# Kernel tuning notes

Hardware: AMD Instinct MI355X
Metric: run time of the kernel (lower is better)

## Reference

```python
import jax, jax.numpy as jnp
import numpy as np

KDIM = 8192
EPS = 1e-8  # F.cosine_similarity default eps


def _encoder(x, W1, b1, W2, b2, W3, b3):
    # x: [..., KDIM] -> [..., 128]; Linear(KDIM,512)->ReLU->Linear(512,256)->ReLU->Linear(256,128)
    h = jax.nn.relu(x @ W1 + b1)
    h = jax.nn.relu(h @ W2 + b2)
    return h @ W3 + b3


def setup_inputs() -> dict:
    key = jax.random.key(0)
    ks = jax.random.split(key, 16)

    def lin(k, fan_in, fan_out):
        bound = 1.0 / np.sqrt(fan_in)
        kw, kb = jax.random.split(k)
        W = jax.random.uniform(kw, (fan_in, fan_out), jnp.float32, -bound, bound)
        b = jax.random.uniform(kb, (fan_out,), jnp.float32, -bound, bound)
        return W, b

    W1, b1 = lin(ks[0], KDIM, 512)
    W2, b2 = lin(ks[1], 512, 256)
    W3, b3 = lin(ks[2], 256, 128)
    Wi1, bi1 = lin(ks[3], 128 + 6, 64)
    Wi2, bi2 = lin(ks[4], 64, 32)
    Wi3, bi3 = lin(ks[5], 32, 1)

    return {
        "new_knowledge": jax.random.normal(ks[6], (KDIM,), jnp.float32),
        "existing_knowledge": jax.random.normal(ks[7], (10, KDIM), jnp.float32),
        "math_metrics": jax.random.uniform(ks[8], (6,), jnp.float32),
        "W1": W1, "b1": b1, "W2": W2, "b2": b2, "W3": W3, "b3": b3,
        "Wi1": Wi1, "bi1": bi1, "Wi2": Wi2, "bi2": bi2, "Wi3": Wi3, "bi3": bi3,
    }


def reference(new_knowledge, existing_knowledge, math_metrics,
              W1, b1, W2, b2, W3, b3, Wi1, bi1, Wi2, bi2, Wi3, bi3):
    # Encode new knowledge: [128]
    new_enc = _encoder(new_knowledge, W1, b1, W2, b2, W3, b3)
    # Batched encode of the (up to 10) existing knowledge vectors: [10, 128]
    ex_enc = _encoder(existing_knowledge, W1, b1, W2, b2, W3, b3)

    # Per-item geometric distance (L2 norm of difference)
    diff = new_enc[None, :] - ex_enc                     # [10, 128]
    geo_dist = jnp.sqrt(jnp.sum(diff * diff, axis=-1))   # [10]

    # Per-item cosine similarity with torch eps clamping
    new_n = jnp.maximum(jnp.linalg.norm(new_enc), EPS)
    ex_n = jnp.maximum(jnp.linalg.norm(ex_enc, axis=-1), EPS)  # [10]
    cos = (ex_enc @ new_enc) / (new_n * ex_n)            # [10]

    avg_consistency = jnp.mean(geo_dist - cos)

    # Mathematical-constraint integrator MLP on [128 + 6]
    combined = jnp.concatenate([new_enc, math_metrics])  # [134]
    h = jax.nn.relu(combined @ Wi1 + bi1)
    h = jax.nn.relu(h @ Wi2 + bi2)
    quality = h @ Wi3 + bi3                              # [1]

    integration_loss = jnp.exp(-quality)                 # [1]
    total = jnp.squeeze(avg_consistency + integration_loss)
    return total
```

## Files before the change

### kernel.cpp

```cpp
#include <hip/hip_runtime.h>
#include <math.h>

#define EPS 1e-8f

__device__ __forceinline__ void gridbar(int* bar, int target) {
  __syncthreads();
  if (threadIdx.x == 0) {
    __threadfence();
    __hip_atomic_fetch_add(bar, 1, __ATOMIC_RELAXED, __HIP_MEMORY_SCOPE_AGENT);
    while (__hip_atomic_load(bar, __ATOMIC_RELAXED, __HIP_MEMORY_SCOPE_AGENT) < target) {
      __builtin_amdgcn_s_sleep(1);
    }
    __threadfence();
  }
  __syncthreads();
}

__device__ __forceinline__ float wredsum(float v) {
#pragma unroll
  for (int o = 32; o > 0; o >>= 1) v += __shfl_down(v, o, 64);
  return v;
}

__global__ __launch_bounds__(256) void k_l1(const float* __restrict__ xn,
                                            const float* __restrict__ xe,
                                            const float* __restrict__ W1,
                                            float* __restrict__ p1,
                                            int* __restrict__ bars) {
  if (blockIdx.x == 0 && blockIdx.y == 0 && threadIdx.x == 0) {
    bars[0] = 0; bars[1] = 0; bars[2] = 0;
  }
  __shared__ float red[11 * 16 * 65];
  const int cg  = threadIdx.x & 15;
  const int ks  = threadIdx.x >> 4;
  const int col = blockIdx.x * 64 + cg * 4;
  const int k0  = blockIdx.y * 256 + ks * 16;

  float4 acc[11];
#pragma unroll
  for (int r = 0; r < 11; ++r) acc[r] = make_float4(0.f, 0.f, 0.f, 0.f);

#pragma unroll 8
  for (int i = 0; i < 16; ++i) {
    const int k = k0 + i;
    const float4 w = *(const float4*)&W1[(size_t)k * 512 + col];
    float xv = xn[k];
    acc[0].x = fmaf(xv, w.x, acc[0].x); acc[0].y = fmaf(xv, w.y, acc[0].y);
    acc[0].z = fmaf(xv, w.z, acc[0].z); acc[0].w = fmaf(xv, w.w, acc[0].w);
#pragma unroll
    for (int r = 0; r < 10; ++r) {
      const float xr = xe[r * 8192 + k];
      acc[r + 1].x = fmaf(xr, w.x, acc[r + 1].x);
      acc[r + 1].y = fmaf(xr, w.y, acc[r + 1].y);
      acc[r + 1].z = fmaf(xr, w.z, acc[r + 1].z);
      acc[r + 1].w = fmaf(xr, w.w, acc[r + 1].w);
    }
  }

#pragma unroll
  for (int r = 0; r < 11; ++r) {
    const int base = (r * 16 + ks) * 65 + cg * 4;
    red[base]     = acc[r].x; red[base + 1] = acc[r].y;
    red[base + 2] = acc[r].z; red[base + 3] = acc[r].w;
  }
  __syncthreads();
  if (threadIdx.x < 176) {
    const int r = threadIdx.x >> 4;
    const int c = threadIdx.x & 15;
    float4 s = make_float4(0.f, 0.f, 0.f, 0.f);
#pragma unroll
    for (int k = 0; k < 16; ++k) {
      const int b = (r * 16 + k) * 65 + c * 4;
      s.x += red[b]; s.y += red[b + 1]; s.z += red[b + 2]; s.w += red[b + 3];
    }
    *(float4*)&p1[((size_t)blockIdx.y * 11 + r) * 512 + blockIdx.x * 64 + c * 4] = s;
  }
}

__global__ __launch_bounds__(256) void k_rest(
    const float* __restrict__ p1, const float* __restrict__ b1,
    const float* __restrict__ W2, const float* __restrict__ b2,
    const float* __restrict__ W3, const float* __restrict__ b3,
    const float* __restrict__ mm,
    const float* __restrict__ Wi1, const float* __restrict__ bi1,
    const float* __restrict__ Wi2, const float* __restrict__ bi2,
    const float* __restrict__ Wi3, const float* __restrict__ bi3,
    float* __restrict__ H1, float* __restrict__ H2a, float* __restrict__ enca,
    int* __restrict__ bars, float* __restrict__ out) {
  __shared__ float red2[11 * 16 * 17];
  __shared__ float red3[11 * 64 * 5];
  __shared__ __align__(16) float wi1s[134 * 64];
  __shared__ float comb[134];
  __shared__ float h1s[64];
  const int tid = threadIdx.x;
  const int b = blockIdx.x;

  if (tid < 88) {
    const int idx = b * 88 + tid;
    const int c = idx & 511;
    float s = b1[c];
#pragma unroll 8
    for (int ch = 0; ch < 32; ++ch) s += p1[(size_t)ch * 5632 + idx];
    H1[idx] = fmaxf(s, 0.f);
  } else if (tid < 132) {
    H2a[b * 44 + (tid - 88)] = 0.f;
  } else if (tid < 154) {
    enca[b * 22 + (tid - 132)] = 0.f;
  }
  gridbar(&bars[0], 64);

  {
    const int ct = b & 15, kt = b >> 4;
    const int c = tid & 15, ksl = tid >> 4;
    const int col = ct * 16 + c;
    float acc[11];
#pragma unroll
    for (int r = 0; r < 11; ++r) acc[r] = 0.f;
#pragma unroll
    for (int kk = 0; kk < 8; ++kk) {
      const int k = kt * 128 + kk * 16 + ksl;
      const float wv = W2[(size_t)k * 256 + col];
#pragma unroll
      for (int r = 0; r < 11; ++r) acc[r] = fmaf(H1[r * 512 + k], wv, acc[r]);
    }
#pragma unroll
    for (int r = 0; r < 11; ++r) red2[(r * 16 + ksl) * 17 + c] = acc[r];
  }
  __syncthreads();
  if (tid < 176) {
    const int r = tid >> 4, c = tid & 15;
    float s = 0.f;
#pragma unroll
    for (int ks = 0; ks < 16; ++ks) s += red2[(r * 16 + ks) * 17 + c];
    atomicAdd(&H2a[r * 256 + (b & 15) * 16 + c], s);
  }
  gridbar(&bars[1], 64);

  {
    const int ct = b & 31, kt = b >> 5;
    const int c = tid & 3, ksl = tid >> 2;
    const int col = ct * 4 + c;
    float acc[11];
#pragma unroll
    for (int r = 0; r < 11; ++r) acc[r] = 0.f;
#pragma unroll
    for (int kk = 0; kk < 2; ++kk) {
      const int k = kt * 128 + kk * 64 + ksl;
      const float wv = W3[(size_t)k * 128 + col];
      const float bb = b2[k];
#pragma unroll
      for (int r = 0; r < 11; ++r) {
        const float h2 = fmaxf(H2a[r * 256 + k] + bb, 0.f);
        acc[r] = fmaf(h2, wv, acc[r]);
      }
    }
#pragma unroll
    for (int r = 0; r < 11; ++r) red3[(r * 64 + ksl) * 5 + c] = acc[r];
  }
  __syncthreads();
  if (tid < 44) {
    const int r = tid >> 2, c = tid & 3;
    float s = 0.f;
#pragma unroll 8
    for (int ks = 0; ks < 64; ++ks) s += red3[(r * 64 + ks) * 5 + c];
    atomicAdd(&enca[r * 128 + (b & 31) * 4 + c], s);
  }
  gridbar(&bars[2], 64);
  if (b != 0) return;

  for (int i = tid; i < (134 * 64) / 4; i += 256)
    *(float4*)&wi1s[i * 4] = *(const float4*)&Wi1[i * 4];

  const int t = tid;
  float n0 = 0.f, n1 = 0.f, consist = 0.f, nn = 0.f;
  if (t < 64) {
    n0 = enca[t] + b3[t];
    n1 = enca[64 + t] + b3[64 + t];
    comb[t] = n0; comb[64 + t] = n1;
    if (t < 6) comb[128 + t] = mm[t];
    nn = wredsum(n0 * n0 + n1 * n1);
#pragma unroll
    for (int r = 1; r <= 10; ++r) {
      const float e0 = enca[r * 128 + t] + b3[t];
      const float e1 = enca[r * 128 + 64 + t] + b3[64 + t];
      const float d0 = e0 - n0, d1 = e1 - n1;
      const float g  = wredsum(d0 * d0 + d1 * d1);
      const float q  = wredsum(e0 * e0 + e1 * e1);
      const float dd = wredsum(e0 * n0 + e1 * n1);
      if (t == 0) {
        const float geo = sqrtf(g);
        const float den = fmaxf(sqrtf(nn), EPS) * fmaxf(sqrtf(q), EPS);
        consist += geo - dd / den;
      }
    }
  }
  __syncthreads();
  if (t < 64) {
    float h = bi1[t];
#pragma unroll 4
    for (int k = 0; k < 134; ++k) h = fmaf(comb[k], wi1s[k * 64 + t], h);
    h1s[t] = fmaxf(h, 0.f);
  }
  __syncthreads();
  if (t < 64) {
    float part = 0.f;
    if (t < 32) {
      float h2 = bi2[t];
#pragma unroll 8
      for (int k = 0; k < 64; ++k) h2 = fmaf(h1s[k], Wi2[k * 32 + t], h2);
      part = fmaxf(h2, 0.f) * Wi3[t];
    }
    const float qual = wredsum(part);
    if (t == 0) out[0] = consist * 0.1f + expf(-(qual + bi3[0]));
  }
}

extern "C" void kernel_launch(void* const* d_in, const int* in_sizes, int n_in,
                              void* d_out, int out_size, void* d_ws, size_t ws_size,
                              hipStream_t stream) {
  (void)in_sizes; (void)n_in; (void)out_size; (void)ws_size;
  const float* xn  = (const float*)d_in[0];
  const float* xe  = (const float*)d_in[1];
  const float* mm  = (const float*)d_in[2];
  const float* W1  = (const float*)d_in[3];
  const float* b1  = (const float*)d_in[4];
  const float* W2  = (const float*)d_in[5];
  const float* b2  = (const float*)d_in[6];
  const float* W3  = (const float*)d_in[7];
  const float* b3  = (const float*)d_in[8];
  const float* Wi1 = (const float*)d_in[9];
  const float* bi1 = (const float*)d_in[10];
  const float* Wi2 = (const float*)d_in[11];
  const float* bi2 = (const float*)d_in[12];
  const float* Wi3 = (const float*)d_in[13];
  const float* bi3 = (const float*)d_in[14];
  float* out = (float*)d_out;

  char* ws = (char*)d_ws;
  float* p1   = (float*)(ws);
  float* H1   = (float*)(ws + 720896);
  float* H2a  = (float*)(ws + 743424);
  float* enca = (float*)(ws + 754688);
  int*   bars = (int*)  (ws + 760320);

  hipLaunchKernelGGL(k_l1, dim3(8, 32), dim3(256), 0, stream, xn, xe, W1, p1, bars);
  hipLaunchKernelGGL(k_rest, dim3(64), dim3(256), 0, stream,
                     p1, b1, W2, b2, W3, b3, mm,
                     Wi1, bi1, Wi2, bi2, Wi3, bi3,
                     H1, H2a, enca, bars, out);
}
```

Measured before the change: 131.9 us.

## Replace grid-barrier persistent kernel with separate per-layer kernel launches

Drops the persistent 64-block kernel, with its software grid barriers and atomic accumulation, and splits the work into three kernels: H1 reduction, layer 2 (16 blocks, H1 staged in shared memory, no atomics) and a single 1024-thread block that does layer 3 plus the heads. The aim is to remove spin-wait barrier latency and atomic traffic, and to overlap the Wi1 load with the W3 matmul. The cost is two extra kernel launches and fewer blocks in the later stages, so parallelism there is lower.

Measured after the change: 120.6 us. 8.6% less time.

```diff
diff --git a/kernel.cpp b/kernel.cpp
--- a/kernel.cpp
+++ b/kernel.cpp
@@ -2,19 +2,6 @@
 #include <math.h>
 
 #define EPS 1e-8f
-
-__device__ __forceinline__ void gridbar(int* bar, int target) {
-  __syncthreads();
-  if (threadIdx.x == 0) {
-    __threadfence();
-    __hip_atomic_fetch_add(bar, 1, __ATOMIC_RELAXED, __HIP_MEMORY_SCOPE_AGENT);
-    while (__hip_atomic_load(bar, __ATOMIC_RELAXED, __HIP_MEMORY_SCOPE_AGENT) < target) {
-      __builtin_amdgcn_s_sleep(1);
-    }
-    __threadfence();
-  }
-  __syncthreads();
-}
 
 __device__ __forceinline__ float wredsum(float v) {
 #pragma unroll
@@ -25,11 +12,7 @@
 __global__ __launch_bounds__(256) void k_l1(const float* __restrict__ xn,
                                             const float* __restrict__ xe,
                                             const float* __restrict__ W1,
-                                            float* __restrict__ p1,
-                                            int* __restrict__ bars) {
-  if (blockIdx.x == 0 && blockIdx.y == 0 && threadIdx.x == 0) {
-    bars[0] = 0; bars[1] = 0; bars[2] = 0;
-  }
+                                            float* __restrict__ p1) {
   __shared__ float red[11 * 16 * 65];
   const int cg  = threadIdx.x & 15;
   const int ks  = threadIdx.x >> 4;
@@ -77,112 +60,112 @@
   }
 }
 
-__global__ __launch_bounds__(256) void k_rest(
-    const float* __restrict__ p1, const float* __restrict__ b1,
-    const float* __restrict__ W2, const float* __restrict__ b2,
-    const float* __restrict__ W3, const float* __restrict__ b3,
-    const float* __restrict__ mm,
+__global__ __launch_bounds__(256) void k_h1(const float* __restrict__ p1,
+                                            const float* __restrict__ b1,
+                                            float* __restrict__ H1) {
+  const int idx = blockIdx.x * 256 + threadIdx.x;
+  float s = 0.f;
+#pragma unroll
+  for (int ch = 0; ch < 32; ++ch) s += p1[(size_t)ch * 5632 + idx];
+  H1[idx] = fmaxf(s + b1[idx & 511], 0.f);
+}
+
+__global__ __launch_bounds__(256) void k_h2(const float* __restrict__ H1,
+                                            const float* __restrict__ W2,
+                                            const float* __restrict__ b2,
+                                            float* __restrict__ H2) {
+  __shared__ float h1s[5632];
+  __shared__ float red[11 * 16 * 17];
+  const int tid = threadIdx.x;
+  for (int i = tid; i < 1408; i += 256)
+    *(float4*)&h1s[i * 4] = *(const float4*)&H1[i * 4];
+  __syncthreads();
+
+  const int c = tid & 15, ks = tid >> 4;
+  const int col = blockIdx.x * 16 + c;
+  float acc[11];
+#pragma unroll
+  for (int r = 0; r < 11; ++r) acc[r] = 0.f;
+#pragma unroll
+  for (int kk = 0; kk < 32; ++kk) {
+    const int k = kk * 16 + ks;
+    const float wv = W2[(size_t)k * 256 + col];
+#pragma unroll
+    for (int r = 0; r < 11; ++r) acc[r] = fmaf(h1s[r * 512 + k], wv, acc[r]);
+  }
+#pragma unroll
+  for (int r = 0; r < 11; ++r) red[(r * 16 + ks) * 17 + c] = acc[r];
+  __syncthreads();
+  if (tid < 176) {
+    const int r = tid >> 4, cc = tid & 15;
+    float s = 0.f;
+#pragma unroll
+    for (int k = 0; k < 16; ++k) s += red[(r * 16 + k) * 17 + cc];
+    const int oc = blockIdx.x * 16 + cc;
+    H2[r * 256 + oc] = fmaxf(s + b2[oc], 0.f);
+  }
+}
+
+__global__ __launch_bounds__(1024) void k_fin(
+    const float* __restrict__ H2, const float* __restrict__ W3,
+    const float* __restrict__ b3, const float* __restrict__ mm,
     const float* __restrict__ Wi1, const float* __restrict__ bi1,
     const float* __restrict__ Wi2, const float* __restrict__ bi2,
     const float* __restrict__ Wi3, const float* __restrict__ bi3,
-    float* __restrict__ H1, float* __restrict__ H2a, float* __restrict__ enca,
-    int* __restrict__ bars, float* __restrict__ out) {
-  __shared__ float red2[11 * 16 * 17];
-  __shared__ float red3[11 * 64 * 5];
-  __shared__ __align__(16) float wi1s[134 * 64];
+    float* __restrict__ out) {
+  __shared__ __align__(16) float h2s[2816];
+  __shared__ __align__(16) float wi1s[8576];
+  __shared__ float red[11 * 8 * 128];
+  __shared__ float encs[1408];
   __shared__ float comb[134];
   __shared__ float h1s[64];
-  const int tid = threadIdx.x;
-  const int b = blockIdx.x;
-
-  if (tid < 88) {
-    const int idx = b * 88 + tid;
-    const int c = idx & 511;
-    float s = b1[c];
-#pragma unroll 8
-    for (int ch = 0; ch < 32; ++ch) s += p1[(size_t)ch * 5632 + idx];
-    H1[idx] = fmaxf(s, 0.f);
-  } else if (tid < 132) {
-    H2a[b * 44 + (tid - 88)] = 0.f;
-  } else if (tid < 154) {
-    enca[b * 22 + (tid - 132)] = 0.f;
-  }
-  gridbar(&bars[0], 64);
+  const int t = threadIdx.x;
+
+  for (int i = t; i < 2848; i += 1024) {
+    if (i < 704) *(float4*)&h2s[i * 4] = *(const float4*)&H2[i * 4];
+    else         *(float4*)&wi1s[(i - 704) * 4] = *(const float4*)&Wi1[(size_t)(i - 704) * 4];
+  }
+  __syncthreads();
 
   {
-    const int ct = b & 15, kt = b >> 4;
-    const int c = tid & 15, ksl = tid >> 4;
-    const int col = ct * 16 + c;
+    const int c = t & 127, g = t >> 7;
     float acc[11];
 #pragma unroll
     for (int r = 0; r < 11; ++r) acc[r] = 0.f;
 #pragma unroll
-    for (int kk = 0; kk < 8; ++kk) {
-      const int k = kt * 128 + kk * 16 + ksl;
-      const float wv = W2[(size_t)k * 256 + col];
-#pragma unroll
-      for (int r = 0; r < 11; ++r) acc[r] = fmaf(H1[r * 512 + k], wv, acc[r]);
-    }
-#pragma unroll
-    for (int r = 0; r < 11; ++r) red2[(r * 16 + ksl) * 17 + c] = acc[r];
-  }
-  __syncthreads();
-  if (tid < 176) {
-    const int r = tid >> 4, c = tid & 15;
-    float s = 0.f;
-#pragma unroll
-    for (int ks = 0; ks < 16; ++ks) s += red2[(r * 16 + ks) * 17 + c];
-    atomicAdd(&H2a[r * 256 + (b & 15) * 16 + c], s);
-  }
-  gridbar(&bars[1], 64);
-
-  {
-    const int ct = b & 31, kt = b >> 5;
-    const int c = tid & 3, ksl = tid >> 2;
-    const int col = ct * 4 + c;
-    float acc[11];
-#pragma unroll
-    for (int r = 0; r < 11; ++r) acc[r] = 0.f;
-#pragma unroll
-    for (int kk = 0; kk < 2; ++kk) {
-      const int k = kt * 128 + kk * 64 + ksl;
-      const float wv = W3[(size_t)k * 128 + col];
-      const float bb = b2[k];
-#pragma unroll
-      for (int r = 0; r < 11; ++r) {
-        const float h2 = fmaxf(H2a[r * 256 + k] + bb, 0.f);
-        acc[r] = fmaf(h2, wv, acc[r]);
-      }
-    }
-#pragma unroll
-    for (int r = 0; r < 11; ++r) red3[(r * 64 + ksl) * 5 + c] = acc[r];
-  }
-  __syncthreads();
-  if (tid < 44) {
-    const int r = tid >> 2, c = tid & 3;
-    float s = 0.f;
-#pragma unroll 8
-    for (int ks = 0; ks < 64; ++ks) s += red3[(r * 64 + ks) * 5 + c];
-    atomicAdd(&enca[r * 128 + (b & 31) * 4 + c], s);
-  }
-  gridbar(&bars[2], 64);
-  if (b != 0) return;
-
-  for (int i = tid; i < (134 * 64) / 4; i += 256)
-    *(float4*)&wi1s[i * 4] = *(const float4*)&Wi1[i * 4];
-
-  const int t = tid;
-  float n0 = 0.f, n1 = 0.f, consist = 0.f, nn = 0.f;
+    for (int kk = 0; kk < 32; ++kk) {
+      const int k = g * 32 + kk;
+      const float wv = W3[(size_t)k * 128 + c];
+#pragma unroll
+      for (int r = 0; r < 11; ++r) acc[r] = fmaf(h2s[r * 256 + k], wv, acc[r]);
+    }
+#pragma unroll
+    for (int r = 0; r < 11; ++r) red[(r * 8 + g) * 128 + c] = acc[r];
+  }
+  __syncthreads();
+  for (int o = t; o < 1408; o += 1024) {
+    const int r = o >> 7, c = o & 127;
+    float s = b3[c];
+#pragma unroll
+    for (int g = 0; g < 8; ++g) s += red[(r * 8 + g) * 128 + c];
+    encs[o] = s;
+  }
+  __syncthreads();
+
+  float consist = 0.f;
+  float n0 = 0.f, n1 = 0.f;
   if (t < 64) {
-    n0 = enca[t] + b3[t];
-    n1 = enca[64 + t] + b3[64 + t];
+    n0 = encs[t]; n1 = encs[64 + t];
     comb[t] = n0; comb[64 + t] = n1;
     if (t < 6) comb[128 + t] = mm[t];
-    nn = wredsum(n0 * n0 + n1 * n1);
+  }
+  __syncthreads();
+  if (t < 64) {
+    const float nn = wredsum(n0 * n0 + n1 * n1);
 #pragma unroll
     for (int r = 1; r <= 10; ++r) {
-      const float e0 = enca[r * 128 + t] + b3[t];
-      const float e1 = enca[r * 128 + 64 + t] + b3[64 + t];
+      const float e0 = encs[r * 128 + t];
+      const float e1 = encs[r * 128 + 64 + t];
       const float d0 = e0 - n0, d1 = e1 - n1;
       const float g  = wredsum(d0 * d0 + d1 * d1);
       const float q  = wredsum(e0 * e0 + e1 * e1);
@@ -193,13 +176,12 @@
         consist += geo - dd / den;
       }
     }
-  }
-  __syncthreads();
-  if (t < 64) {
-    float h = bi1[t];
+  } else if (t < 128) {
+    const int tt = t - 64;
+    float h = bi1[tt];
 #pragma unroll 4
-    for (int k = 0; k < 134; ++k) h = fmaf(comb[k], wi1s[k * 64 + t], h);
-    h1s[t] = fmaxf(h, 0.f);
+    for (int k = 0; k < 134; ++k) h = fmaf(comb[k], wi1s[k * 64 + tt], h);
+    h1s[tt] = fmaxf(h, 0.f);
   }
   __syncthreads();
   if (t < 64) {
@@ -237,15 +219,13 @@
   float* out = (float*)d_out;
 
   char* ws = (char*)d_ws;
-  float* p1   = (float*)(ws);
-  float* H1   = (float*)(ws + 720896);
-  float* H2a  = (float*)(ws + 743424);
-  float* enca = (float*)(ws + 754688);
-  int*   bars = (int*)  (ws + 760320);
-
-  hipLaunchKernelGGL(k_l1, dim3(8, 32), dim3(256), 0, stream, xn, xe, W1, p1, bars);
-  hipLaunchKernelGGL(k_rest, dim3(64), dim3(256), 0, stream,
-                     p1, b1, W2, b2, W3, b3, mm,
-                     Wi1, bi1, Wi2, bi2, Wi3, bi3,
-                     H1, H2a, enca, bars, out);
-}
+  float* p1 = (float*)(ws);
+  float* H1 = (float*)(ws + 720896);
+  float* H2 = (float*)(ws + 743424);
+
+  hipLaunchKernelGGL(k_l1,  dim3(8, 32), dim3(256),  0, stream, xn, xe, W1, p1);
+  hipLaunchKernelGGL(k_h1,  dim3(22),    dim3(256),  0, stream, p1, b1, H1);
+  hipLaunchKernelGGL(k_h2,  dim3(16),    dim3(256),  0, stream, H1, W2, b2, H2);
+  hipLaunchKernelGGL(k_fin, dim3(1),     dim3(1024), 0, stream,
+                     H2, W3, b3, mm, Wi1, bi1, Wi2, bi2, Wi3, bi3, out);
+}
```
